# Kernel optimization log

Measured on AMD Instinct MI355X. Metric: run time of the kernel, lower is better.

## Reference

```python
import jax, jax.numpy as jnp
import numpy as np

NC, NS, NX, NZ = 128, 2048, 256, 512
B, K = 4, 1
NNZ = NX * NZ * NC  # 16_777_216 nonzeros (~Nc contributions per pixel)


def setup_inputs() -> dict:
    key = jax.random.key(0)
    k1, k2, k3, k4 = jax.random.split(key, 4)
    x = jax.random.normal(k1, (B, K, NC, NS), dtype=jnp.float32)
    csr_vals = jax.random.normal(k2, (NNZ,), dtype=jnp.float32)
    csr_rows = jnp.sort(jax.random.randint(k3, (NNZ,), 0, NX * NZ, dtype=jnp.int64))
    csr_cols = jax.random.randint(k4, (NNZ,), 0, NS * NC, dtype=jnp.int64)
    return {"x": x, "csr_vals": csr_vals, "csr_rows": csr_rows, "csr_cols": csr_cols}


def reference(x, csr_vals, csr_rows, csr_cols):
    # (B,K,Nc,Ns) -> (B,K,Ns,Nc) -> (B*K, Ns*Nc) -> transpose -> (Ns*Nc, B*K)
    rhs = jnp.transpose(x, (0, 1, 3, 2)).reshape(B * K, NS * NC).T
    # SpMM in COO form: out[r, :] += vals * rhs[cols, :]
    gathered = csr_vals[:, None] * rhs[csr_cols]          # (nnz, B*K)
    img_vec = jax.ops.segment_sum(gathered, csr_rows, num_segments=NX * NZ)  # (Nx*Nz, B*K)
    # transpose -> (B*K, Nx*Nz) -> (B,K,Nx,Nz) -> (B,K,Nz,Nx)
    return jnp.transpose(img_vec.T.reshape(B, K, NX, NZ), (0, 1, 3, 2))
```

## Files before the change

### kernel.cpp

```cpp
#include <hip/hip_runtime.h>

#define NC 128
#define NS 2048
#define NX 256
#define NZ 512
#define NB 4
#define NROWS (NX * NZ)
#define NCOLS (NS * NC)


__global__ void pack_rhs_kernel(const float* __restrict__ x,
                                float4* __restrict__ rhs) {
    int j = blockIdx.x * blockDim.x + threadIdx.x;
    if (j >= NCOLS) return;
    int c = j & (NC - 1);
    int s = j >> 7;
    int base = c * NS + s;
    float4 v;
    v.x = x[base];
    v.y = x[base + 1 * NC * NS];
    v.z = x[base + 2 * NC * NS];
    v.w = x[base + 3 * NC * NS];
    rhs[j] = v;
}

__global__ void row_bounds_kernel(const int* __restrict__ rows, int nnz,
                                  int* __restrict__ row_start) {
    int r = blockIdx.x * blockDim.x + threadIdx.x;
    if (r > NROWS) return;
    int lo = 0, hi = nnz;
    while (lo < hi) {
        int mid = (lo + hi) >> 1;
        if (rows[mid] < r) lo = mid + 1;
        else hi = mid;
    }
    row_start[r] = lo;
}

__global__ void __launch_bounds__(256) spmm_kernel(
        const float* __restrict__ vals,
        const int* __restrict__ cols,
        const int* __restrict__ row_start,
        const float4* __restrict__ rhs,
        float* __restrict__ out) {
    int r = (blockIdx.x << 2) + (threadIdx.x >> 6);
    int lane = threadIdx.x & 63;
    int start = row_start[r];
    int end   = row_start[r + 1];

    float4 acc = {0.f, 0.f, 0.f, 0.f};
    for (int i = start + lane; i < end; i += 64) {
        float v = vals[i];
        int col = cols[i];
        float4 rv = rhs[col];
        acc.x += v * rv.x;
        acc.y += v * rv.y;
        acc.z += v * rv.z;
        acc.w += v * rv.w;
    }

    #pragma unroll
    for (int off = 32; off >= 1; off >>= 1) {
        acc.x += __shfl_xor(acc.x, off, 64);
        acc.y += __shfl_xor(acc.y, off, 64);
        acc.z += __shfl_xor(acc.z, off, 64);
        acc.w += __shfl_xor(acc.w, off, 64);
    }

    if (lane < 4) {
        float o = (lane == 0) ? acc.x : (lane == 1) ? acc.y
                : (lane == 2) ? acc.z : acc.w;
        int ix = r >> 9;
        int iz = r & (NZ - 1);
        out[lane * NROWS + iz * NX + ix] = o;
    }
}

__global__ void __launch_bounds__(256) spmm_direct_kernel(
        const float* __restrict__ x,
        const float* __restrict__ vals,
        const int* __restrict__ rows,
        const int* __restrict__ cols,
        int nnz,
        float* __restrict__ out) {
    int r = (blockIdx.x << 2) + (threadIdx.x >> 6);
    int lane = threadIdx.x & 63;

    int start, end;
    {
        int lo = 0, hi = nnz;
        while (lo < hi) { int mid = (lo + hi) >> 1; if (rows[mid] < r) lo = mid + 1; else hi = mid; }
        start = lo;
        hi = nnz;
        int key = r + 1;
        while (lo < hi) { int mid = (lo + hi) >> 1; if (rows[mid] < key) lo = mid + 1; else hi = mid; }
        end = lo;
    }

    float4 acc = {0.f, 0.f, 0.f, 0.f};
    for (int i = start + lane; i < end; i += 64) {
        float v = vals[i];
        int col = cols[i];
        int c = col & (NC - 1);
        int s = col >> 7;
        int base = c * NS + s;
        acc.x += v * x[base];
        acc.y += v * x[base + 1 * NC * NS];
        acc.z += v * x[base + 2 * NC * NS];
        acc.w += v * x[base + 3 * NC * NS];
    }

    #pragma unroll
    for (int off = 32; off >= 1; off >>= 1) {
        acc.x += __shfl_xor(acc.x, off, 64);
        acc.y += __shfl_xor(acc.y, off, 64);
        acc.z += __shfl_xor(acc.z, off, 64);
        acc.w += __shfl_xor(acc.w, off, 64);
    }

    if (lane < 4) {
        float o = (lane == 0) ? acc.x : (lane == 1) ? acc.y
                : (lane == 2) ? acc.z : acc.w;
        int ix = r >> 9;
        int iz = r & (NZ - 1);
        out[lane * NROWS + iz * NX + ix] = o;
    }
}

extern "C" void kernel_launch(void* const* d_in, const int* in_sizes, int n_in,
                              void* d_out, int out_size, void* d_ws, size_t ws_size,
                              hipStream_t stream) {
    const float* x        = (const float*)d_in[0];
    const float* csr_vals = (const float*)d_in[1];
    const int*   csr_rows = (const int*)d_in[2];
    const int*   csr_cols = (const int*)d_in[3];
    float* out = (float*)d_out;
    int nnz = in_sizes[1];

    size_t need = (size_t)NCOLS * sizeof(float4) + (size_t)(NROWS + 1) * sizeof(int);
    if (ws_size >= need) {
        float4* rhs       = (float4*)d_ws;
        int*    row_start = (int*)((char*)d_ws + (size_t)NCOLS * sizeof(float4));
        pack_rhs_kernel<<<(NCOLS + 255) / 256, 256, 0, stream>>>(x, rhs);
        row_bounds_kernel<<<(NROWS + 1 + 255) / 256, 256, 0, stream>>>(csr_rows, nnz, row_start);
        spmm_kernel<<<NROWS / 4, 256, 0, stream>>>(csr_vals, csr_cols, row_start, rhs, out);
    } else {
        spmm_direct_kernel<<<NROWS / 4, 256, 0, stream>>>(x, csr_vals, csr_rows, csr_cols, nnz, out);
    }
}
```

Baseline: 307.5 us.

## Assign eight rows per wavefront with 8-lane groups and nontemporal loads

```diff
diff --git a/kernel.cpp b/kernel.cpp
--- a/kernel.cpp
+++ b/kernel.cpp
@@ -43,15 +43,20 @@
         const int* __restrict__ row_start,
         const float4* __restrict__ rhs,
         float* __restrict__ out) {
-    int r = (blockIdx.x << 2) + (threadIdx.x >> 6);
+    int wid  = (blockIdx.x << 2) + (threadIdx.x >> 6);
     int lane = threadIdx.x & 63;
-    int start = row_start[r];
-    int end   = row_start[r + 1];
+    int g = lane >> 3;
+    int t = lane & 7;
+
+    int rb = 0;
+    if (lane < 9) rb = row_start[(wid << 3) + lane];
+    int s = __shfl(rb, g);
+    int e = __shfl(rb, g + 1);
 
     float4 acc = {0.f, 0.f, 0.f, 0.f};
-    for (int i = start + lane; i < end; i += 64) {
-        float v = vals[i];
-        int col = cols[i];
+    for (int i = s + t; i < e; i += 8) {
+        float v  = __builtin_nontemporal_load(vals + i);
+        int  col = __builtin_nontemporal_load(cols + i);
         float4 rv = rhs[col];
         acc.x += v * rv.x;
         acc.y += v * rv.y;
@@ -60,19 +65,19 @@
     }
 
     #pragma unroll
-    for (int off = 32; off >= 1; off >>= 1) {
-        acc.x += __shfl_xor(acc.x, off, 64);
-        acc.y += __shfl_xor(acc.y, off, 64);
-        acc.z += __shfl_xor(acc.z, off, 64);
-        acc.w += __shfl_xor(acc.w, off, 64);
+    for (int off = 4; off >= 1; off >>= 1) {
+        acc.x += __shfl_xor(acc.x, off, 8);
+        acc.y += __shfl_xor(acc.y, off, 8);
+        acc.z += __shfl_xor(acc.z, off, 8);
+        acc.w += __shfl_xor(acc.w, off, 8);
     }
 
-    if (lane < 4) {
-        float o = (lane == 0) ? acc.x : (lane == 1) ? acc.y
-                : (lane == 2) ? acc.z : acc.w;
+    if (t < 4) {
+        int r = (wid << 3) + g;
+        float o = (t == 0) ? acc.x : (t == 1) ? acc.y : (t == 2) ? acc.z : acc.w;
         int ix = r >> 9;
         int iz = r & (NZ - 1);
-        out[lane * NROWS + iz * NX + ix] = o;
+        out[t * NROWS + iz * NX + ix] = o;
     }
 }
 
@@ -85,7 +90,6 @@
         float* __restrict__ out) {
     int r = (blockIdx.x << 2) + (threadIdx.x >> 6);
     int lane = threadIdx.x & 63;
-
     int start, end;
     {
         int lo = 0, hi = nnz;
@@ -96,20 +100,18 @@
         while (lo < hi) { int mid = (lo + hi) >> 1; if (rows[mid] < key) lo = mid + 1; else hi = mid; }
         end = lo;
     }
-
     float4 acc = {0.f, 0.f, 0.f, 0.f};
     for (int i = start + lane; i < end; i += 64) {
         float v = vals[i];
         int col = cols[i];
         int c = col & (NC - 1);
-        int s = col >> 7;
-        int base = c * NS + s;
+        int sidx = col >> 7;
+        int base = c * NS + sidx;
         acc.x += v * x[base];
         acc.y += v * x[base + 1 * NC * NS];
         acc.z += v * x[base + 2 * NC * NS];
         acc.w += v * x[base + 3 * NC * NS];
     }
-
     #pragma unroll
     for (int off = 32; off >= 1; off >>= 1) {
         acc.x += __shfl_xor(acc.x, off, 64);
@@ -117,10 +119,8 @@
         acc.z += __shfl_xor(acc.z, off, 64);
         acc.w += __shfl_xor(acc.w, off, 64);
     }
-
     if (lane < 4) {
-        float o = (lane == 0) ? acc.x : (lane == 1) ? acc.y
-                : (lane == 2) ? acc.z : acc.w;
+        float o = (lane == 0) ? acc.x : (lane == 1) ? acc.y : (lane == 2) ? acc.z : acc.w;
         int ix = r >> 9;
         int iz = r & (NZ - 1);
         out[lane * NROWS + iz * NX + ix] = o;
@@ -143,7 +143,7 @@
         int*    row_start = (int*)((char*)d_ws + (size_t)NCOLS * sizeof(float4));
         pack_rhs_kernel<<<(NCOLS + 255) / 256, 256, 0, stream>>>(x, rhs);
         row_bounds_kernel<<<(NROWS + 1 + 255) / 256, 256, 0, stream>>>(csr_rows, nnz, row_start);
-        spmm_kernel<<<NROWS / 4, 256, 0, stream>>>(csr_vals, csr_cols, row_start, rhs, out);
+        spmm_kernel<<<NROWS / 8 / 4, 256, 0, stream>>>(csr_vals, csr_cols, row_start, rhs, out);
     } else {
         spmm_direct_kernel<<<NROWS / 4, 256, 0, stream>>>(x, csr_vals, csr_rows, csr_cols, nnz, out);
     }
```

After: 372.5 us. +21.1%, slower.

## Replace row-parallel CSR SpMM with nnz-parallel segmented runs, fp16 RHS and atomics

Applied to the files above, without the earlier changes.

```diff
diff --git a/kernel.cpp b/kernel.cpp
--- a/kernel.cpp
+++ b/kernel.cpp
@@ -1,79 +1,106 @@
 #include <hip/hip_runtime.h>
+#include <hip/hip_fp16.h>
 
 #define NC 128
 #define NS 2048
 #define NX 256
 #define NZ 512
-#define NB 4
 #define NROWS (NX * NZ)
 #define NCOLS (NS * NC)
+#define RUN 16
 
 
+struct alignas(8) Half4 { __half2 lo, hi; };
+
 __global__ void pack_rhs_kernel(const float* __restrict__ x,
-                                float4* __restrict__ rhs) {
+                                Half4* __restrict__ rhs) {
     int j = blockIdx.x * blockDim.x + threadIdx.x;
     if (j >= NCOLS) return;
     int c = j & (NC - 1);
     int s = j >> 7;
     int base = c * NS + s;
-    float4 v;
-    v.x = x[base];
-    v.y = x[base + 1 * NC * NS];
-    v.z = x[base + 2 * NC * NS];
-    v.w = x[base + 3 * NC * NS];
-    rhs[j] = v;
+    Half4 h;
+    h.lo = __float22half2_rn(make_float2(x[base],              x[base + 1 * NC * NS]));
+    h.hi = __float22half2_rn(make_float2(x[base + 2 * NC * NS], x[base + 3 * NC * NS]));
+    rhs[j] = h;
 }
 
-__global__ void row_bounds_kernel(const int* __restrict__ rows, int nnz,
-                                  int* __restrict__ row_start) {
-    int r = blockIdx.x * blockDim.x + threadIdx.x;
-    if (r > NROWS) return;
-    int lo = 0, hi = nnz;
-    while (lo < hi) {
-        int mid = (lo + hi) >> 1;
-        if (rows[mid] < r) lo = mid + 1;
-        else hi = mid;
-    }
-    row_start[r] = lo;
+__device__ __forceinline__ void flush_row(float* __restrict__ out, int r, float4 a) {
+    int ix = r >> 9;
+    int iz = r & (NZ - 1);
+    int o = iz * NX + ix;
+    atomicAdd(&out[0 * NROWS + o], a.x);
+    atomicAdd(&out[1 * NROWS + o], a.y);
+    atomicAdd(&out[2 * NROWS + o], a.z);
+    atomicAdd(&out[3 * NROWS + o], a.w);
 }
 
-__global__ void __launch_bounds__(256) spmm_kernel(
+__global__ void __launch_bounds__(256) spmm_runs_kernel(
         const float* __restrict__ vals,
         const int* __restrict__ cols,
-        const int* __restrict__ row_start,
-        const float4* __restrict__ rhs,
-        float* __restrict__ out) {
-    int r = (blockIdx.x << 2) + (threadIdx.x >> 6);
-    int lane = threadIdx.x & 63;
-    int start = row_start[r];
-    int end   = row_start[r + 1];
+        const int* __restrict__ rows,
+        const Half4* __restrict__ rhs,
+        float* __restrict__ out,
+        int nnz) {
+    int gid = blockIdx.x * blockDim.x + threadIdx.x;
+    int base = gid * RUN;
+    if (base >= nnz) return;
 
-    float4 acc = {0.f, 0.f, 0.f, 0.f};
-    for (int i = start + lane; i < end; i += 64) {
-        float v = vals[i];
-        int col = cols[i];
-        float4 rv = rhs[col];
-        acc.x += v * rv.x;
-        acc.y += v * rv.y;
-        acc.z += v * rv.z;
-        acc.w += v * rv.w;
+    float4 v[4];
+    int4   c[4], r[4];
+    if (base + RUN <= nnz) {
+        #pragma unroll
+        for (int q = 0; q < 4; ++q) {
+            v[q] = *(const float4*)(vals + base + 4 * q);
+            c[q] = *(const int4*)(cols + base + 4 * q);
+            r[q] = *(const int4*)(rows + base + 4 * q);
+        }
+    } else {
+        #pragma unroll
+        for (int q = 0; q < 4; ++q) {
+            v[q] = make_float4(0.f, 0.f, 0.f, 0.f);
+            c[q] = make_int4(0, 0, 0, 0);
+            r[q] = make_int4(0, 0, 0, 0);
+            #pragma unroll
+            for (int k = 0; k < 4; ++k) {
+                int e = base + 4 * q + k;
+                if (e < nnz) {
+                    (&v[q].x)[k] = vals[e];
+                    (&c[q].x)[k] = cols[e];
+                    (&r[q].x)[k] = rows[e];
+                }
+            }
+        }
     }
 
+    Half4 g[RUN];
     #pragma unroll
-    for (int off = 32; off >= 1; off >>= 1) {
-        acc.x += __shfl_xor(acc.x, off, 64);
-        acc.y += __shfl_xor(acc.y, off, 64);
-        acc.z += __shfl_xor(acc.z, off, 64);
-        acc.w += __shfl_xor(acc.w, off, 64);
+    for (int q = 0; q < 4; ++q) {
+        g[4 * q + 0] = rhs[c[q].x];
+        g[4 * q + 1] = rhs[c[q].y];
+        g[4 * q + 2] = rhs[c[q].z];
+        g[4 * q + 3] = rhs[c[q].w];
     }
 
-    if (lane < 4) {
-        float o = (lane == 0) ? acc.x : (lane == 1) ? acc.y
-                : (lane == 2) ? acc.z : acc.w;
-        int ix = r >> 9;
-        int iz = r & (NZ - 1);
-        out[lane * NROWS + iz * NX + ix] = o;
+    int cur = r[0].x;
+    float4 acc = make_float4(0.f, 0.f, 0.f, 0.f);
+    #pragma unroll
+    for (int j = 0; j < RUN; ++j) {
+        int   rj = (&r[j >> 2].x)[j & 3];
+        float vj = (&v[j >> 2].x)[j & 3];
+        float2 lo = __half22float2(g[j].lo);
+        float2 hi = __half22float2(g[j].hi);
+        if (rj != cur) {
+            flush_row(out, cur, acc);
+            acc = make_float4(0.f, 0.f, 0.f, 0.f);
+            cur = rj;
+        }
+        acc.x += vj * lo.x;
+        acc.y += vj * lo.y;
+        acc.z += vj * hi.x;
+        acc.w += vj * hi.y;
     }
+    flush_row(out, cur, acc);
 }
 
 __global__ void __launch_bounds__(256) spmm_direct_kernel(
@@ -85,7 +112,6 @@
         float* __restrict__ out) {
     int r = (blockIdx.x << 2) + (threadIdx.x >> 6);
     int lane = threadIdx.x & 63;
-
     int start, end;
     {
         int lo = 0, hi = nnz;
@@ -96,20 +122,18 @@
         while (lo < hi) { int mid = (lo + hi) >> 1; if (rows[mid] < key) lo = mid + 1; else hi = mid; }
         end = lo;
     }
-
     float4 acc = {0.f, 0.f, 0.f, 0.f};
     for (int i = start + lane; i < end; i += 64) {
         float v = vals[i];
         int col = cols[i];
-        int c = col & (NC - 1);
-        int s = col >> 7;
-        int base = c * NS + s;
-        acc.x += v * x[base];
-        acc.y += v * x[base + 1 * NC * NS];
-        acc.z += v * x[base + 2 * NC * NS];
-        acc.w += v * x[base + 3 * NC * NS];
+        int cc = col & (NC - 1);
+        int ss = col >> 7;
+        int b = cc * NS + ss;
+        acc.x += v * x[b];
+        acc.y += v * x[b + 1 * NC * NS];
+        acc.z += v * x[b + 2 * NC * NS];
+        acc.w += v * x[b + 3 * NC * NS];
     }
-
     #pragma unroll
     for (int off = 32; off >= 1; off >>= 1) {
         acc.x += __shfl_xor(acc.x, off, 64);
@@ -117,10 +141,8 @@
         acc.z += __shfl_xor(acc.z, off, 64);
         acc.w += __shfl_xor(acc.w, off, 64);
     }
-
     if (lane < 4) {
-        float o = (lane == 0) ? acc.x : (lane == 1) ? acc.y
-                : (lane == 2) ? acc.z : acc.w;
+        float o = (lane == 0) ? acc.x : (lane == 1) ? acc.y : (lane == 2) ? acc.z : acc.w;
         int ix = r >> 9;
         int iz = r & (NZ - 1);
         out[lane * NROWS + iz * NX + ix] = o;
@@ -137,13 +159,15 @@
     float* out = (float*)d_out;
     int nnz = in_sizes[1];
 
-    size_t need = (size_t)NCOLS * sizeof(float4) + (size_t)(NROWS + 1) * sizeof(int);
+    size_t need = (size_t)NCOLS * sizeof(Half4);
     if (ws_size >= need) {
-        float4* rhs       = (float4*)d_ws;
-        int*    row_start = (int*)((char*)d_ws + (size_t)NCOLS * sizeof(float4));
+        Half4* rhs = (Half4*)d_ws;
+        hipMemsetAsync(out, 0, (size_t)out_size * sizeof(float), stream);
         pack_rhs_kernel<<<(NCOLS + 255) / 256, 256, 0, stream>>>(x, rhs);
-        row_bounds_kernel<<<(NROWS + 1 + 255) / 256, 256, 0, stream>>>(csr_rows, nnz, row_start);
-        spmm_kernel<<<NROWS / 4, 256, 0, stream>>>(csr_vals, csr_cols, row_start, rhs, out);
+        int nthreads = (nnz + RUN - 1) / RUN;
+        int nblocks  = (nthreads + 255) / 256;
+        spmm_runs_kernel<<<nblocks, 256, 0, stream>>>(csr_vals, csr_cols, csr_rows,
+                                                      rhs, out, nnz);
     } else {
         spmm_direct_kernel<<<NROWS / 4, 256, 0, stream>>>(x, csr_vals, csr_rows, csr_cols, nnz, out);
     }
```

Result: slower. 395.8 us (+28.7%).
